# Optimization experiments

Hardware: AMD Instinct MI355X
Metric: run time of the kernel (lower is better)

The kernel has to match this reference:

```python
import jax, jax.numpy as jnp
import numpy as np

N_NODES = 100000
N_EDGES = 1600000
N_GRAPHS = 512


def gcn_conv(x, row, col, W, b):
    # x: [N, Cin], row/col: [E] (self-loops already appended)
    n = x.shape[0]
    h = x @ W                                        # [N, Cout]
    deg = jax.ops.segment_sum(jnp.ones_like(col, dtype=x.dtype), col, num_segments=n)
    dinv = jnp.where(deg > 0, deg ** -0.5, 0.0)
    norm = dinv[row] * dinv[col]                     # [E]
    msg = norm[:, None] * h[row]                     # [E, Cout]
    out = jax.ops.segment_sum(msg, col, num_segments=n)
    return out + b


def setup_inputs() -> dict:
    key = jax.random.key(0)
    ks = jax.random.split(key, 10)
    x = jax.random.normal(ks[0], (N_NODES, 128), dtype=jnp.float32)
    edge_index = jax.random.randint(ks[1], (2, N_EDGES), 0, N_NODES, dtype=jnp.int64)
    batch = jnp.sort(jax.random.randint(ks[2], (N_NODES,), 0, N_GRAPHS, dtype=jnp.int64))
    def lin_w(k, fan_in, fan_out):
        bound = 1.0 / np.sqrt(fan_in)
        return jax.random.uniform(k, (fan_in, fan_out), jnp.float32, -bound, bound)
    # GCN layers (bias zero-initialized per reset_parameters)
    W1 = lin_w(ks[3], 128, 128); b1 = jnp.zeros((128,), jnp.float32)
    W2 = lin_w(ks[4], 128, 128); b2 = jnp.zeros((128,), jnp.float32)
    # MLP layers (Linear with bias)
    Wm1 = lin_w(ks[5], 128, 64)
    bm1 = jax.random.uniform(ks[6], (64,), jnp.float32, -1/np.sqrt(128), 1/np.sqrt(128))
    Wm2 = lin_w(ks[7], 64, 1)
    bm2 = jax.random.uniform(ks[8], (1,), jnp.float32, -1/np.sqrt(64), 1/np.sqrt(64))
    return {"x": x, "edge_index": edge_index, "batch": batch,
            "W1": W1, "b1": b1, "W2": W2, "b2": b2,
            "Wm1": Wm1, "bm1": bm1, "Wm2": Wm2, "bm2": bm2}


def reference(x, edge_index, batch, W1, b1, W2, b2, Wm1, bm1, Wm2, bm2):
    n = x.shape[0]
    loops = jnp.arange(n, dtype=edge_index.dtype)
    row = jnp.concatenate([edge_index[0], loops])
    col = jnp.concatenate([edge_index[1], loops])
    # GCN: conv -> relu -> conv
    h = gcn_conv(x, row, col, W1, b1)
    h = jax.nn.relu(h)
    h = gcn_conv(h, row, col, W2, b2)
    # scatter-mean pooling over graphs
    sums = jax.ops.segment_sum(h, batch, num_segments=N_GRAPHS)      # [G, C]
    counts = jax.ops.segment_sum(jnp.ones((n,), h.dtype), batch, num_segments=N_GRAPHS)
    g = sums / jnp.maximum(counts, 1.0)[:, None]
    # MLP: linear -> relu -> linear
    g = jax.nn.relu(g @ Wm1 + bm1)
    out = g @ Wm2 + bm2
    return out
```

## Files before the change

### kernel.cpp

```cpp
#include <hip/hip_runtime.h>
#include <math.h>

#define C_DIM 128
#define POOL_CHUNK 64
#define BKT_SHIFT 7
#define MAX_B 1024
#define CB 256
#define FB_CAP 8192
typedef unsigned short ushort_t;
typedef __attribute__((ext_vector_type(8))) short short8;
typedef __attribute__((ext_vector_type(4))) float f32x4;

static inline int ceil_div(int a, int b) { return (a + b - 1) / b; }

__device__ inline ushort_t f2bf(float f) {
    union { float f; unsigned u; } v; v.f = f;
    unsigned r = v.u + 0x7FFFu + ((v.u >> 16) & 1u);
    return (ushort_t)(r >> 16);
}
__device__ inline float bf2f(unsigned s) {
    union { unsigned u; float f; } v; v.u = s << 16; return v.f;
}
__device__ inline float bf_lo(unsigned u) {
    union { unsigned v; float f; } c; c.v = u << 16; return c.f;
}
__device__ inline float bf_hi(unsigned u) {
    union { unsigned v; float f; } c; c.v = u & 0xFFFF0000u; return c.f;
}
__device__ inline void accum8(uint4 u, float acc[8]) {
    acc[0] += bf_lo(u.x); acc[1] += bf_hi(u.x);
    acc[2] += bf_lo(u.y); acc[3] += bf_hi(u.y);
    acc[4] += bf_lo(u.z); acc[5] += bf_hi(u.z);
    acc[6] += bf_lo(u.w); acc[7] += bf_hi(u.w);
}


__global__ __launch_bounds__(256) void k_bcount(
    const int* __restrict__ col, int E, int chunk, int B,
    int* __restrict__ counts,
    const float* __restrict__ W1, const float* __restrict__ W2,
    uint4* __restrict__ wf1, uint4* __restrict__ wf2,
    float* __restrict__ gsums, int GC, int* __restrict__ cursor) {
    int t = threadIdx.x, blk = blockIdx.x;
    if (blk >= CB) {
        const float* W = (blk == CB) ? W1 : W2;
        uint4* wf = (blk == CB) ? wf1 : wf2;
        for (int f = t; f < 2048; f += 256) {
            int lane = f & 63, kkn = f >> 6;
            int kk = kkn & 3, nt = kkn >> 2;
            int n = lane & 15, quad = lane >> 4;
            union { ushort_t h[8]; uint4 v; } u;
#pragma unroll
            for (int j = 0; j < 8; ++j)
                u.h[j] = f2bf(W[(size_t)(kk * 32 + quad * 8 + j) * C_DIM + nt * 16 + n]);
            wf[f] = u.v;
        }
        return;
    }
    for (int i = blk * 256 + t; i < GC; i += CB * 256) gsums[i] = 0.f;
    if (blk == 0 && t == 0) *cursor = 0;

    __shared__ int hist[MAX_B];
    for (int i = t; i < B; i += 256) hist[i] = 0;
    __syncthreads();
    int s = blk * chunk;
    int e = s + chunk; if (e > E) e = E;
    for (int i = s + 4 * t; i < e; i += 1024) {
        int4 c = *(const int4*)(col + i);
        atomicAdd(&hist[c.x >> BKT_SHIFT], 1);
        atomicAdd(&hist[c.y >> BKT_SHIFT], 1);
        atomicAdd(&hist[c.z >> BKT_SHIFT], 1);
        atomicAdd(&hist[c.w >> BKT_SHIFT], 1);
    }
    __syncthreads();
    for (int i = t; i < B; i += 256)
        counts[(size_t)i * CB + blk] = hist[i];
}

__global__ __launch_bounds__(CB) void k_bscan(
    int* __restrict__ counts, int* __restrict__ bbase, int* __restrict__ btot,
    int* __restrict__ cursor) {
    __shared__ int sd[CB];
    int b = blockIdx.x, t = threadIdx.x;
    int v = counts[(size_t)b * CB + t];
    sd[t] = v;
    __syncthreads();
    for (int off = 1; off < CB; off <<= 1) {
        int x = (t >= off) ? sd[t - off] : 0;
        __syncthreads();
        sd[t] += x;
        __syncthreads();
    }
    counts[(size_t)b * CB + t] = sd[t] - v;
    if (t == CB - 1) {
        btot[b] = sd[CB - 1];
        bbase[b] = atomicAdd(cursor, sd[CB - 1]);
    }
}

__global__ __launch_bounds__(256) void k_bscatter(
    const int* __restrict__ row, const int* __restrict__ col, int E, int chunk,
    int B, const int* __restrict__ counts, const int* __restrict__ bbase,
    int* __restrict__ epk) {
    __shared__ int cur[MAX_B];
    int t = threadIdx.x, blk = blockIdx.x;
    for (int i = t; i < B; i += 256)
        cur[i] = bbase[i] + counts[(size_t)i * CB + blk];
    __syncthreads();
    int s = blk * chunk;
    int e = s + chunk; if (e > E) e = E;
    for (int i = s + 4 * t; i < e; i += 1024) {
        int4 c = *(const int4*)(col + i);
        int4 r = *(const int4*)(row + i);
        int s0 = atomicAdd(&cur[c.x >> BKT_SHIFT], 1); epk[s0] = (r.x << 7) | (c.x & 127);
        int s1 = atomicAdd(&cur[c.y >> BKT_SHIFT], 1); epk[s1] = (r.y << 7) | (c.y & 127);
        int s2 = atomicAdd(&cur[c.z >> BKT_SHIFT], 1); epk[s2] = (r.z << 7) | (c.z & 127);
        int s3 = atomicAdd(&cur[c.w >> BKT_SHIFT], 1); epk[s3] = (r.w << 7) | (c.w & 127);
    }
}

__global__ __launch_bounds__(256) void k_bfinal(
    const int* __restrict__ epk, const int* __restrict__ bbase,
    const int* __restrict__ btot, int N,
    int2* __restrict__ offs2, float* __restrict__ dinv, int* __restrict__ csr) {
    __shared__ int sh[FB_CAP];
    __shared__ int cnt[128];
    __shared__ int pre[128];
    __shared__ int cur[128];
    int bkt = blockIdx.x, t = threadIdx.x;
    int s = bbase[bkt];
    int m = btot[bkt];
    int e = s + m;
    int base = bkt << BKT_SHIFT;
    int nn = N - base; if (nn > 128) nn = 128;
    bool fits = (m <= FB_CAP);
    if (t < 128) cnt[t] = 0;
    __syncthreads();
    if (fits) {
        for (int i = t; i < m; i += 256) {
            int u = epk[s + i];
            sh[i] = u;
            atomicAdd(&cnt[u & 127], 1);
        }
    } else {
        for (int i = s + t; i < e; i += 256)
            atomicAdd(&cnt[epk[i] & 127], 1);
    }
    __syncthreads();
    if (t < 128) pre[t] = cnt[t];
    __syncthreads();
    for (int off = 1; off < 128; off <<= 1) {
        int x = (t >= off && t < 128) ? pre[t - off] : 0;
        __syncthreads();
        if (t < 128) pre[t] += x;
        __syncthreads();
    }
    if (t < 128) {
        int ex = pre[t] - cnt[t];
        cur[t] = ex;
        if (t < nn) {
            offs2[base + t] = make_int2(s + ex, s + ex + cnt[t]);
            dinv[base + t] = 1.0f / sqrtf((float)cnt[t] + 1.0f);
        }
    }
    __syncthreads();
    if (fits) {
        for (int i = t; i < m; i += 256) {
            int u = sh[i];
            int slot = atomicAdd(&cur[u & 127], 1);
            csr[s + slot] = u >> 7;
        }
    } else {
        for (int i = s + t; i < e; i += 256) {
            int u = epk[i];
            int slot = atomicAdd(&cur[u & 127], 1);
            csr[s + slot] = u >> 7;
        }
    }
}

template <int ABF16>
__global__ __launch_bounds__(256) void k_matmul_mfma(
    const float* __restrict__ Af, const ushort_t* __restrict__ Abf,
    const uint4* __restrict__ wfrag, const float* __restrict__ dinv,
    ushort_t* __restrict__ Cb, int N) {
    __shared__ uint4 wfs[2048];
    __shared__ __align__(16) ushort_t As[64 * 136];
    int t = threadIdx.x;
    int wv = t >> 6, lane = t & 63;
    int n = lane & 15, quad = lane >> 4;
    int row0 = blockIdx.x * 64;

    for (int i = t; i < 2048; i += 256) wfs[i] = wfrag[i];

    if (ABF16) {
#pragma unroll
        for (int i = 0; i < 4; ++i) {
            int idx = i * 256 + t;
            int r = idx >> 4, c8 = idx & 15;
            int grow = row0 + r; if (grow >= N) grow = N - 1;
            uint4 u = *(const uint4*)(Abf + (size_t)grow * C_DIM + c8 * 8);
            *(uint4*)&As[r * 136 + c8 * 8] = u;
        }
    } else {
#pragma unroll
        for (int i = 0; i < 8; ++i) {
            int idx = i * 256 + t;
            int r = idx >> 5, cq = idx & 31;
            int grow = row0 + r; if (grow >= N) grow = N - 1;
            float4 f = *(const float4*)(Af + (size_t)grow * C_DIM + cq * 4);
            union { ushort_t h[4]; uint2 v; } c;
            c.h[0] = f2bf(f.x); c.h[1] = f2bf(f.y);
            c.h[2] = f2bf(f.z); c.h[3] = f2bf(f.w);
            *(uint2*)&As[r * 136 + cq * 4] = c.v;
        }
    }

    f32x4 acc[8];
#pragma unroll
    for (int i = 0; i < 8; ++i) acc[i] = (f32x4){0.f, 0.f, 0.f, 0.f};

    __syncthreads();

    int rl = wv * 16 + n;
#pragma unroll
    for (int kk = 0; kk < 4; ++kk) {
        union { uint4 v; short8 s; } ca;
        ca.v = *(const uint4*)&As[rl * 136 + kk * 32 + quad * 8];
#pragma unroll
        for (int nt = 0; nt < 8; ++nt) {
            union { uint4 v; short8 s; } cb;
            cb.v = wfs[(nt * 4 + kk) * 64 + lane];
            acc[nt] = __builtin_amdgcn_mfma_f32_16x16x32_bf16(ca.s, cb.s, acc[nt], 0, 0, 0);
        }
    }

    __syncthreads();
#pragma unroll
    for (int reg = 0; reg < 4; ++reg) {
        int lr = wv * 16 + quad * 4 + reg;
        int grow = row0 + lr;
        float sc = dinv[grow < N ? grow : N - 1];
#pragma unroll
        for (int nt = 0; nt < 8; ++nt)
            As[lr * 136 + nt * 16 + n] = f2bf(acc[nt][reg] * sc);
    }
    __syncthreads();
    int rows = N - row0; if (rows > 64) rows = 64;
    for (int idx = t; idx < 16 * 64; idx += 256) {
        int r = idx >> 4, c8 = idx & 15;
        if (r < rows)
            *(uint4*)(Cb + (size_t)(row0 + r) * C_DIM + c8 * 8) =
                *(const uint4*)&As[r * 136 + c8 * 8];
    }
}

template <int RELU>
__global__ __launch_bounds__(256) void k_aggregate(
    const ushort_t* __restrict__ hs, const int2* __restrict__ offs2,
    const int* __restrict__ csr, const float* __restrict__ dinv,
    const float* __restrict__ bias, uint4* __restrict__ outV, int N) {
    int node = (blockIdx.x << 2) + (threadIdx.x >> 6);
    if (node >= N) return;
    int t = threadIdx.x & 63;
    int q = t >> 4;
    int fs = t & 15;
    int2 se = offs2[node];
    int s = se.x, e = se.y;

    float acc[8];
    {
        uint4 u = *(const uint4*)(hs + (size_t)node * C_DIM + fs * 8);
        float v[8];
        v[0] = bf_lo(u.x); v[1] = bf_hi(u.x);
        v[2] = bf_lo(u.y); v[3] = bf_hi(u.y);
        v[4] = bf_lo(u.z); v[5] = bf_hi(u.z);
        v[6] = bf_lo(u.w); v[7] = bf_hi(u.w);
#pragma unroll
        for (int i = 0; i < 8; ++i) acc[i] = (q == 0) ? v[i] : 0.f;
    }

    int j = s;
    for (; j + 16 <= e; j += 16) {
        int r[4];
#pragma unroll
        for (int b = 0; b < 4; ++b) r[b] = csr[j + b * 4 + q];
        uint4 u[4];
#pragma unroll
        for (int b = 0; b < 4; ++b)
            u[b] = *(const uint4*)(hs + (size_t)r[b] * C_DIM + fs * 8);
#pragma unroll
        for (int b = 0; b < 4; ++b) accum8(u[b], acc);
    }
    for (; j + 4 <= e; j += 4) {
        int r = csr[j + q];
        uint4 u = *(const uint4*)(hs + (size_t)r * C_DIM + fs * 8);
        accum8(u, acc);
    }
    if (j + q < e) {
        int r = csr[j + q];
        uint4 u = *(const uint4*)(hs + (size_t)r * C_DIM + fs * 8);
        accum8(u, acc);
    }

#pragma unroll
    for (int i = 0; i < 8; ++i) {
        acc[i] += __shfl_xor(acc[i], 16);
        acc[i] += __shfl_xor(acc[i], 32);
    }

    if (q == 0) {
        float dn = dinv[node];
        float4 b0 = *(const float4*)(bias + fs * 8);
        float4 b1 = *(const float4*)(bias + fs * 8 + 4);
        float o[8];
        o[0] = dn * acc[0] + b0.x; o[1] = dn * acc[1] + b0.y;
        o[2] = dn * acc[2] + b0.z; o[3] = dn * acc[3] + b0.w;
        o[4] = dn * acc[4] + b1.x; o[5] = dn * acc[5] + b1.y;
        o[6] = dn * acc[6] + b1.z; o[7] = dn * acc[7] + b1.w;
        if (RELU) {
#pragma unroll
            for (int i = 0; i < 8; ++i) o[i] = fmaxf(o[i], 0.f);
        }
        uint4 pk;
        pk.x = (unsigned)f2bf(o[0]) | ((unsigned)f2bf(o[1]) << 16);
        pk.y = (unsigned)f2bf(o[2]) | ((unsigned)f2bf(o[3]) << 16);
        pk.z = (unsigned)f2bf(o[4]) | ((unsigned)f2bf(o[5]) << 16);
        pk.w = (unsigned)f2bf(o[6]) | ((unsigned)f2bf(o[7]) << 16);
        outV[(size_t)node * 16 + fs] = pk;
    }
}

__global__ __launch_bounds__(128) void k_pool_sum(
    const ushort_t* __restrict__ h, const int* __restrict__ batch, int n,
    float* __restrict__ sums) {
    int r0 = blockIdx.x * POOL_CHUNK;
    int r1 = r0 + POOL_CHUNK; if (r1 > n) r1 = n;
    if (r0 >= n) return;
    int t = threadIdx.x;
    int c = t & 63, rr = t >> 6;
    float2 acc = make_float2(0.f, 0.f);
    int g = batch[r0];
    int i = r0;
    while (i < r1) {
        if (i + 8 <= r1 && batch[i + 7] == g) {
#pragma unroll
            for (int b = 0; b < 4; ++b) {
                unsigned u = *(const unsigned*)(h + (size_t)(i + rr + 2 * b) * C_DIM + c * 2);
                acc.x += bf_lo(u); acc.y += bf_hi(u);
            }
            i += 8;
        } else {
            int bi = batch[i];
            if (bi != g) {
                atomicAdd(&sums[(size_t)g * C_DIM + c * 2], acc.x);
                atomicAdd(&sums[(size_t)g * C_DIM + c * 2 + 1], acc.y);
                acc = make_float2(0.f, 0.f); g = bi;
            }
            if (rr == 0) {
                unsigned u = *(const unsigned*)(h + (size_t)i * C_DIM + c * 2);
                acc.x += bf_lo(u); acc.y += bf_hi(u);
            }
            ++i;
        }
    }
    atomicAdd(&sums[(size_t)g * C_DIM + c * 2], acc.x);
    atomicAdd(&sums[(size_t)g * C_DIM + c * 2 + 1], acc.y);
}

__global__ __launch_bounds__(128) void k_mlp(
    const float* __restrict__ sums, const int* __restrict__ batch, int n,
    const float* __restrict__ Wm1, const float* __restrict__ bm1,
    const float* __restrict__ Wm2, const float* __restrict__ bm2,
    float* __restrict__ out) {
    int g = blockIdx.x;
    int t = threadIdx.x;
    int lo = 0, hi = n;
    while (lo < hi) { int m = (lo + hi) >> 1; if (batch[m] < g) lo = m + 1; else hi = m; }
    int start = lo;
    lo = start; hi = n;
    while (lo < hi) { int m = (lo + hi) >> 1; if (batch[m] < g + 1) lo = m + 1; else hi = m; }
    float cnt = (float)(lo - start);

    float mean = sums[(size_t)g * C_DIM + t] / fmaxf(cnt, 1.0f);

    __shared__ float m_s[128];
    __shared__ float hid[64];
    m_s[t] = mean;
    __syncthreads();
    if (t < 64) {
        float a = bm1[t];
#pragma unroll 4
        for (int k = 0; k < 128; ++k) a += m_s[k] * Wm1[k * 64 + t];
        hid[t] = fmaxf(a, 0.f) * Wm2[t];
    }
    __syncthreads();
    if (t < 64) {
        float v = hid[t];
        for (int off = 32; off > 0; off >>= 1) v += __shfl_down(v, off);
        if (t == 0) out[g] = v + bm2[0];
    }
}

extern "C" void kernel_launch(void* const* d_in, const int* in_sizes, int n_in,
                              void* d_out, int out_size, void* d_ws, size_t ws_size,
                              hipStream_t stream) {
    const float* x     = (const float*)d_in[0];
    const int*   eidx  = (const int*)d_in[1];
    const int*   batch = (const int*)d_in[2];
    const float* W1    = (const float*)d_in[3];
    const float* b1    = (const float*)d_in[4];
    const float* W2    = (const float*)d_in[5];
    const float* b2    = (const float*)d_in[6];
    const float* Wm1   = (const float*)d_in[7];
    const float* bm1   = (const float*)d_in[8];
    const float* Wm2   = (const float*)d_in[9];
    const float* bm2   = (const float*)d_in[10];

    const int N = in_sizes[2];
    const int E = in_sizes[1] / 2;
    const int G = out_size;
    const int B = (N + 127) >> BKT_SHIFT;

    char* p = (char*)d_ws;
    auto carve = [&](size_t bytes) {
        char* q = p;
        p += (bytes + 255) & ~(size_t)255;
        return q;
    };
    ushort_t* bufT   = (ushort_t*)carve((size_t)N * C_DIM * sizeof(ushort_t));
    ushort_t* bufA   = (ushort_t*)carve((size_t)N * C_DIM * sizeof(ushort_t));
    float*    dinv   = (float*)   carve((size_t)N * sizeof(float));
    int2*     offs2  = (int2*)    carve((size_t)N * sizeof(int2));
    int*      csr    = (int*)     carve((size_t)E * sizeof(int));
    int*      counts = (int*)     carve((size_t)B * CB * sizeof(int));
    int*      btot   = (int*)     carve((size_t)B * sizeof(int));
    int*      bbase  = (int*)     carve((size_t)B * sizeof(int));
    float*    gsums  = (float*)   carve((size_t)G * C_DIM * sizeof(float));
    uint4*    wf1    = (uint4*)   carve(2048 * sizeof(uint4));
    uint4*    wf2    = (uint4*)   carve(2048 * sizeof(uint4));
    int*      cursor = (int*)     carve(sizeof(int));
    int*      epk    = (int*)bufT;

    const int* erow = eidx;
    const int* ecol = eidx + E;
    const int chunk = (ceil_div(E, CB) + 3) & ~3;

    k_bcount<<<CB + 2, 256, 0, stream>>>(ecol, E, chunk, B, counts,
                                         W1, W2, wf1, wf2, gsums, G * C_DIM, cursor);
    k_bscan<<<B, CB, 0, stream>>>(counts, bbase, btot, cursor);
    k_bscatter<<<CB, 256, 0, stream>>>(erow, ecol, E, chunk, B, counts, bbase, epk);
    k_bfinal<<<B, 256, 0, stream>>>(epk, bbase, btot, N, offs2, dinv, csr);

    k_matmul_mfma<0><<<ceil_div(N, 64), 256, 0, stream>>>(x, nullptr, wf1, dinv, bufT, N);
    k_aggregate<1><<<ceil_div(N, 4), 256, 0, stream>>>(bufT, offs2, csr, dinv, b1,
                                                       (uint4*)bufA, N);
    k_matmul_mfma<1><<<ceil_div(N, 64), 256, 0, stream>>>(nullptr, bufA, wf2, dinv, bufT, N);
    k_aggregate<0><<<ceil_div(N, 4), 256, 0, stream>>>(bufT, offs2, csr, dinv, b2,
                                                       (uint4*)bufA, N);
    k_pool_sum<<<ceil_div(N, POOL_CHUNK), 128, 0, stream>>>(bufA, batch, N, gsums);
    k_mlp<<<G, 128, 0, stream>>>(gsums, batch, N, Wm1, bm1, Wm2, bm2, (float*)d_out);
}
```

Baseline: 324.0 us.

## Sort edges locally per chunk in LDS, drop global scatter pass

The count and scatter kernels are merged into one: each block histograms its edge chunk, scans it locally, and buckets the packed edges in shared memory before writing them back contiguously. This replaces the scattered global writes with coalesced ones and removes one kernel launch. The final bucket kernel now gathers its segments from the 256 per-chunk runs, one run per thread, with a serial inner loop. That uneven per-thread loop and the larger shared memory footprint (a 6400-entry sorted array) may lower occupancy.

```diff
diff --git a/kernel.cpp b/kernel.cpp
--- a/kernel.cpp
+++ b/kernel.cpp
@@ -6,6 +6,7 @@
 #define BKT_SHIFT 7
 #define MAX_B 1024
 #define CB 256
+#define CHUNK_MAX 6400
 #define FB_CAP 8192
 typedef unsigned short ushort_t;
 typedef __attribute__((ext_vector_type(8))) short short8;
@@ -35,9 +36,10 @@
 }
 
 
-__global__ __launch_bounds__(256) void k_bcount(
-    const int* __restrict__ col, int E, int chunk, int B,
-    int* __restrict__ counts,
+__global__ __launch_bounds__(256) void k_sortchunk(
+    const int* __restrict__ row, const int* __restrict__ col, int E, int chunk,
+    int B, int* __restrict__ counts, int* __restrict__ sstart,
+    int* __restrict__ epk,
     const float* __restrict__ W1, const float* __restrict__ W2,
     uint4* __restrict__ wf1, uint4* __restrict__ wf2,
     float* __restrict__ gsums, int GC, int* __restrict__ cursor) {
@@ -61,6 +63,10 @@
     if (blk == 0 && t == 0) *cursor = 0;
 
     __shared__ int hist[MAX_B];
+    __shared__ int hscan[MAX_B];
+    __shared__ int sd[256];
+    __shared__ int sorted[CHUNK_MAX];
+
     for (int i = t; i < B; i += 256) hist[i] = 0;
     __syncthreads();
     int s = blk * chunk;
@@ -73,78 +79,110 @@
         atomicAdd(&hist[c.w >> BKT_SHIFT], 1);
     }
     __syncthreads();
-    for (int i = t; i < B; i += 256)
-        counts[(size_t)i * CB + blk] = hist[i];
-}
-
-__global__ __launch_bounds__(CB) void k_bscan(
-    int* __restrict__ counts, int* __restrict__ bbase, int* __restrict__ btot,
-    int* __restrict__ cursor) {
+    {
+        int base4 = t * 4;
+        int vv[4]; int sum = 0;
+#pragma unroll
+        for (int j = 0; j < 4; ++j) {
+            int idx = base4 + j;
+            vv[j] = (idx < B) ? hist[idx] : 0;
+            sum += vv[j];
+        }
+        sd[t] = sum;
+        __syncthreads();
+        for (int off = 1; off < 256; off <<= 1) {
+            int x = (t >= off) ? sd[t - off] : 0;
+            __syncthreads();
+            sd[t] += x;
+            __syncthreads();
+        }
+        int run = sd[t] - sum;
+#pragma unroll
+        for (int j = 0; j < 4; ++j) {
+            int idx = base4 + j;
+            if (idx < B) hscan[idx] = run;
+            run += vv[j];
+        }
+    }
+    __syncthreads();
+    for (int i = t; i < B; i += 256) {
+        counts[(size_t)blk * MAX_B + i] = hist[i];
+        sstart[(size_t)blk * MAX_B + i] = hscan[i];
+    }
+    __syncthreads();
+    for (int i = t; i < B; i += 256) hist[i] = hscan[i];
+    __syncthreads();
+    for (int i = s + 4 * t; i < e; i += 1024) {
+        int4 c = *(const int4*)(col + i);
+        int4 r = *(const int4*)(row + i);
+        int p0 = atomicAdd(&hist[c.x >> BKT_SHIFT], 1); sorted[p0] = (r.x << 7) | (c.x & 127);
+        int p1 = atomicAdd(&hist[c.y >> BKT_SHIFT], 1); sorted[p1] = (r.y << 7) | (c.y & 127);
+        int p2 = atomicAdd(&hist[c.z >> BKT_SHIFT], 1); sorted[p2] = (r.z << 7) | (c.z & 127);
+        int p3 = atomicAdd(&hist[c.w >> BKT_SHIFT], 1); sorted[p3] = (r.w << 7) | (c.w & 127);
+    }
+    __syncthreads();
+    int cnt = e - s;
+    for (int i = t; i < cnt; i += 256) epk[s + i] = sorted[i];
+}
+
+__global__ __launch_bounds__(CB) void k_btotred(
+    const int* __restrict__ counts, int* __restrict__ bbase,
+    int* __restrict__ btot, int* __restrict__ cursor) {
     __shared__ int sd[CB];
     int b = blockIdx.x, t = threadIdx.x;
-    int v = counts[(size_t)b * CB + t];
-    sd[t] = v;
-    __syncthreads();
-    for (int off = 1; off < CB; off <<= 1) {
+    sd[t] = counts[(size_t)t * MAX_B + b];
+    __syncthreads();
+    for (int off = CB / 2; off > 0; off >>= 1) {
+        if (t < off) sd[t] += sd[t + off];
+        __syncthreads();
+    }
+    if (t == 0) {
+        int tot = sd[0];
+        btot[b] = tot;
+        bbase[b] = atomicAdd(cursor, tot);
+    }
+}
+
+__global__ __launch_bounds__(256) void k_bfinal(
+    const int* __restrict__ epk, const int* __restrict__ counts,
+    const int* __restrict__ sstart, const int* __restrict__ bbase,
+    const int* __restrict__ btot, int chunk, int N,
+    int2* __restrict__ offs2, float* __restrict__ dinv, int* __restrict__ csr) {
+    __shared__ int sh[FB_CAP];
+    __shared__ int sd[256];
+    __shared__ int cnt[128];
+    __shared__ int pre[128];
+    __shared__ int cur[128];
+    int bkt = blockIdx.x, t = threadIdx.x;
+    int sbase = bbase[bkt];
+    int m = btot[bkt];
+    int base = bkt << BKT_SHIFT;
+    int nn = N - base; if (nn > 128) nn = 128;
+
+    int segln = counts[(size_t)t * MAX_B + bkt];
+    int gs = t * chunk + sstart[(size_t)t * MAX_B + bkt];
+    sd[t] = segln;
+    __syncthreads();
+    for (int off = 1; off < 256; off <<= 1) {
         int x = (t >= off) ? sd[t - off] : 0;
         __syncthreads();
         sd[t] += x;
         __syncthreads();
     }
-    counts[(size_t)b * CB + t] = sd[t] - v;
-    if (t == CB - 1) {
-        btot[b] = sd[CB - 1];
-        bbase[b] = atomicAdd(cursor, sd[CB - 1]);
-    }
-}
-
-__global__ __launch_bounds__(256) void k_bscatter(
-    const int* __restrict__ row, const int* __restrict__ col, int E, int chunk,
-    int B, const int* __restrict__ counts, const int* __restrict__ bbase,
-    int* __restrict__ epk) {
-    __shared__ int cur[MAX_B];
-    int t = threadIdx.x, blk = blockIdx.x;
-    for (int i = t; i < B; i += 256)
-        cur[i] = bbase[i] + counts[(size_t)i * CB + blk];
-    __syncthreads();
-    int s = blk * chunk;
-    int e = s + chunk; if (e > E) e = E;
-    for (int i = s + 4 * t; i < e; i += 1024) {
-        int4 c = *(const int4*)(col + i);
-        int4 r = *(const int4*)(row + i);
-        int s0 = atomicAdd(&cur[c.x >> BKT_SHIFT], 1); epk[s0] = (r.x << 7) | (c.x & 127);
-        int s1 = atomicAdd(&cur[c.y >> BKT_SHIFT], 1); epk[s1] = (r.y << 7) | (c.y & 127);
-        int s2 = atomicAdd(&cur[c.z >> BKT_SHIFT], 1); epk[s2] = (r.z << 7) | (c.z & 127);
-        int s3 = atomicAdd(&cur[c.w >> BKT_SHIFT], 1); epk[s3] = (r.w << 7) | (c.w & 127);
-    }
-}
-
-__global__ __launch_bounds__(256) void k_bfinal(
-    const int* __restrict__ epk, const int* __restrict__ bbase,
-    const int* __restrict__ btot, int N,
-    int2* __restrict__ offs2, float* __restrict__ dinv, int* __restrict__ csr) {
-    __shared__ int sh[FB_CAP];
-    __shared__ int cnt[128];
-    __shared__ int pre[128];
-    __shared__ int cur[128];
-    int bkt = blockIdx.x, t = threadIdx.x;
-    int s = bbase[bkt];
-    int m = btot[bkt];
-    int e = s + m;
-    int base = bkt << BKT_SHIFT;
-    int nn = N - base; if (nn > 128) nn = 128;
+    int place = sd[t] - segln;
+
     bool fits = (m <= FB_CAP);
     if (t < 128) cnt[t] = 0;
     __syncthreads();
     if (fits) {
-        for (int i = t; i < m; i += 256) {
-            int u = epk[s + i];
-            sh[i] = u;
+        for (int j = 0; j < segln; ++j) {
+            int u = epk[gs + j];
+            sh[place + j] = u;
             atomicAdd(&cnt[u & 127], 1);
         }
     } else {
-        for (int i = s + t; i < e; i += 256)
-            atomicAdd(&cnt[epk[i] & 127], 1);
+        for (int j = 0; j < segln; ++j)
+            atomicAdd(&cnt[epk[gs + j] & 127], 1);
     }
     __syncthreads();
     if (t < 128) pre[t] = cnt[t];
@@ -159,7 +197,7 @@
         int ex = pre[t] - cnt[t];
         cur[t] = ex;
         if (t < nn) {
-            offs2[base + t] = make_int2(s + ex, s + ex + cnt[t]);
+            offs2[base + t] = make_int2(sbase + ex, sbase + ex + cnt[t]);
             dinv[base + t] = 1.0f / sqrtf((float)cnt[t] + 1.0f);
         }
     }
@@ -168,13 +206,13 @@
         for (int i = t; i < m; i += 256) {
             int u = sh[i];
             int slot = atomicAdd(&cur[u & 127], 1);
-            csr[s + slot] = u >> 7;
+            csr[sbase + slot] = u >> 7;
         }
     } else {
-        for (int i = s + t; i < e; i += 256) {
-            int u = epk[i];
+        for (int j = 0; j < segln; ++j) {
+            int u = epk[gs + j];
             int slot = atomicAdd(&cur[u & 127], 1);
-            csr[s + slot] = u >> 7;
+            csr[sbase + slot] = u >> 7;
         }
     }
 }
@@ -433,7 +471,8 @@
     float*    dinv   = (float*)   carve((size_t)N * sizeof(float));
     int2*     offs2  = (int2*)    carve((size_t)N * sizeof(int2));
     int*      csr    = (int*)     carve((size_t)E * sizeof(int));
-    int*      counts = (int*)     carve((size_t)B * CB * sizeof(int));
+    int*      counts = (int*)     carve((size_t)CB * MAX_B * sizeof(int));
+    int*      sstart = (int*)     carve((size_t)CB * MAX_B * sizeof(int));
     int*      btot   = (int*)     carve((size_t)B * sizeof(int));
     int*      bbase  = (int*)     carve((size_t)B * sizeof(int));
     float*    gsums  = (float*)   carve((size_t)G * C_DIM * sizeof(float));
@@ -446,11 +485,12 @@
     const int* ecol = eidx + E;
     const int chunk = (ceil_div(E, CB) + 3) & ~3;
 
-    k_bcount<<<CB + 2, 256, 0, stream>>>(ecol, E, chunk, B, counts,
-                                         W1, W2, wf1, wf2, gsums, G * C_DIM, cursor);
-    k_bscan<<<B, CB, 0, stream>>>(counts, bbase, btot, cursor);
-    k_bscatter<<<CB, 256, 0, stream>>>(erow, ecol, E, chunk, B, counts, bbase, epk);
-    k_bfinal<<<B, 256, 0, stream>>>(epk, bbase, btot, N, offs2, dinv, csr);
+    k_sortchunk<<<CB + 2, 256, 0, stream>>>(erow, ecol, E, chunk, B,
+                                            counts, sstart, epk,
+                                            W1, W2, wf1, wf2, gsums, G * C_DIM, cursor);
+    k_btotred<<<B, CB, 0, stream>>>(counts, bbase, btot, cursor);
+    k_bfinal<<<B, 256, 0, stream>>>(epk, counts, sstart, bbase, btot, chunk, N,
+                                    offs2, dinv, csr);
 
     k_matmul_mfma<0><<<ceil_div(N, 64), 256, 0, stream>>>(x, nullptr, wf1, dinv, bufT, N);
     k_aggregate<1><<<ceil_div(N, 4), 256, 0, stream>>>(bufT, offs2, csr, dinv, b1,
```

Measured after the change: 318.5 us. No clear change (-1.7%).
